# Optimization experiments

Hardware: AMD Instinct MI355X
Metric: run time of the kernel (lower is better)

Reference implementation:

```python
import jax, jax.numpy as jnp
import numpy as np

N = 100_000   # active voxels
CIN = 64
COUT = 64
K = 3
L = 128       # voxel grid extent per axis
C = K // 2    # kernel center


def _offsets():
    # spatial offsets (z, y, x) for all non-center kernel taps, in the same
    # enumeration order as the original module's triple loop
    offs = []
    for dz in range(K):
        for dy in range(K):
            for dx in range(K):
                if (dz, dy, dx) != (C, C, C):
                    offs.append((dz - C, dy - C, dx - C))
    return offs


def _build_neighbor_map(coords):
    # coords: [N,3] int, unique. For each offset build (out_idx, in_idx) pairs
    # where voxel out_idx has an active neighbor in_idx at coords+offset.
    keys = (coords[:, 0].astype(np.int64) * L + coords[:, 1]) * L + coords[:, 2]
    order = np.argsort(keys)
    skeys = keys[order]
    pairs = []
    for (z, y, x) in _offsets():
        nb = coords + np.array([z, y, x], dtype=coords.dtype)
        valid = np.all((nb >= 0) & (nb < L), axis=1)
        nkeys = (nb[:, 0].astype(np.int64) * L + nb[:, 1]) * L + nb[:, 2]
        pos = np.clip(np.searchsorted(skeys, nkeys), 0, N - 1)
        found = valid & (skeys[pos] == nkeys)
        out_idx = np.nonzero(found)[0].astype(np.int32)
        in_idx = order[pos[found]].astype(np.int32)
        pairs.append((out_idx, in_idx))
    P = max(len(o) for o, _ in pairs)
    nei = np.zeros((len(pairs), P, 2), dtype=np.int32)
    sizes = np.zeros(len(pairs), dtype=np.int32)
    for i, (o, j) in enumerate(pairs):
        nei[i, :len(o), 0] = o
        nei[i, :len(o), 1] = j
        sizes[i] = len(o)
    return nei, sizes


def setup_inputs() -> dict:
    rng = np.random.default_rng(0)
    flat = rng.choice(L * L * L, size=N, replace=False)  # unique voxel coords
    coords = np.stack([flat // (L * L), (flat // L) % L, flat % L], axis=1).astype(np.int32)
    nei, sizes = _build_neighbor_map(coords)
    key = jax.random.key(0)
    k1, k2, k3 = jax.random.split(key, 3)
    sp_values = jax.random.normal(k1, (N, CIN), dtype=jnp.float32)
    weight = jax.random.normal(k2, (COUT, K, K, K, CIN), dtype=jnp.float32) * 0.05
    bias = jax.random.normal(k3, (COUT,), dtype=jnp.float32)
    return {"sp_values": sp_values, "weight": weight, "bias": bias,
            "nei_indices": jnp.asarray(nei), "nei_sizes": jnp.asarray(sizes)}


def reference(sp_values, weight, bias, nei_indices, nei_sizes):
    # weight: [Cout,kz,ky,kx,Cin] -> [kz,ky,kx,Cin,Cout] (matches torch permute)
    w = jnp.transpose(weight, (1, 2, 3, 4, 0))
    out = sp_values @ w[C, C, C]                                   # center tap: [N,Cout]
    offs = _offsets()
    w_offs = jnp.stack([w[z + C, y + C, x + C] for (z, y, x) in offs])  # [O,Cin,Cout]
    P = nei_indices.shape[1]
    valid = (jnp.arange(P)[None, :] < nei_sizes[:, None]).astype(sp_values.dtype)  # [O,P]
    gathered = sp_values[nei_indices[:, :, 1]] * valid[:, :, None]  # [O,P,Cin], padded rows zeroed
    contrib = jnp.einsum('opc,ocd->opd', gathered, w_offs)          # [O,P,Cout]
    out = out.at[nei_indices[:, :, 0].reshape(-1)].add(contrib.reshape(-1, out.shape[1]))
    return out + bias
```

## Files before the change

### kernel.cpp

```cpp
#include <hip/hip_runtime.h>
#include <hip/hip_bf16.h>


typedef __bf16 bf16x8 __attribute__((ext_vector_type(8)));
typedef float f32x4 __attribute__((ext_vector_type(4)));

#define TROWS 128
#define WSTR 72

__device__ __forceinline__ unsigned short f2bf(float f) {
    union { float f; unsigned int u; } v; v.f = f;
    unsigned int u = v.u;
    return (unsigned short)((u + 0x7FFFu + ((u >> 16) & 1u)) >> 16);
}
__device__ __forceinline__ ushort4 cvt4(float4 v) {
    ushort4 b;
    b.x = f2bf(v.x); b.y = f2bf(v.y); b.z = f2bf(v.z); b.w = f2bf(v.w);
    return b;
}

__global__ __launch_bounds__(256) void sp3d_prep(
    const float* __restrict__ w, const int* __restrict__ nei,
    const int* __restrict__ sizes, unsigned short* __restrict__ wbf,
    int* __restrict__ starts, int P, int T, int wblocks)
{
    const int b = blockIdx.x;
    if (b < wblocks) {
        int id = b * 256 + threadIdx.x;
        if (id < 27 * 64 * 16) {
            int k4 = id & 15, n = (id >> 4) & 63, tap = id >> 10;
            float4 v = *(const float4*)&w[n * 1728 + tap * 64 + k4 * 4];
            *(ushort4*)&wbf[(tap * 64 + n) * 64 + k4 * 4] = cvt4(v);
        }
    } else {
        int id = (b - wblocks) * 256 + threadIdx.x;
        if (id < 26 * (T + 1)) {
            int t = id % (T + 1), o = id / (T + 1);
            int target = t * TROWS;
            int lo = 0, hi = sizes[o];
            while (lo < hi) {
                int mid = (lo + hi) >> 1;
                if (nei[(o * P + mid) * 2] < target) lo = mid + 1; else hi = mid;
            }
            starts[o * (T + 1) + t] = lo;
        }
    }
}

__device__ __forceinline__ bf16x8 pack8(float4 a, float4 b) {
    union { __hip_bfloat162 h[4]; bf16x8 v; } u;
    u.h[0] = __float22bfloat162_rn(float2{a.x, a.y});
    u.h[1] = __float22bfloat162_rn(float2{a.z, a.w});
    u.h[2] = __float22bfloat162_rn(float2{b.x, b.y});
    u.h[3] = __float22bfloat162_rn(float2{b.z, b.w});
    return u.v;
}

__device__ __forceinline__ void stage_w(unsigned short* dst, const unsigned short* wbf,
                                        int tap, int t) {
    int n = t >> 2, kc = (t & 3) << 4;
    const uint4* src = (const uint4*)&wbf[(tap * 64 + n) * 64 + kc];
    uint4 a = src[0], b = src[1];
    *(uint4*)&dst[n * WSTR + kc] = a;
    *(uint4*)&dst[n * WSTR + kc + 8] = b;
}

__global__ __launch_bounds__(256, 4) void sp3d_main(
    const float* __restrict__ sp, const float* __restrict__ bias,
    const int* __restrict__ nei, const unsigned short* __restrict__ wbf,
    const int* __restrict__ starts, float* __restrict__ out,
    int N, int P, int T)
{
    __shared__ unsigned short Wbuf[2][64 * WSTR];
    __shared__ int tbl[27 * TROWS];
    __shared__ int sOff[27];
    __shared__ int sLo[26];

    const int t = threadIdx.x;
    const int w = t >> 6, lane = t & 63, ml = lane & 15, quad = lane >> 4;
    const int bid = blockIdx.x, row0 = bid * TROWS;

    for (int i = t; i < 27 * TROWS; i += 256) tbl[i] = -1;
    if (t < TROWS) { int r = row0 + t; tbl[13 * TROWS + t] = (r < N) ? r : -1; }
    if (t < 64) {
        int o = t, lo = 0, cnt = 0;
        if (o < 26) {
            lo = starts[o * (T + 1) + bid];
            cnt = starts[o * (T + 1) + bid + 1] - lo;
            sLo[o] = lo;
        }
        int x = cnt;
        #pragma unroll
        for (int d = 1; d < 32; d <<= 1) {
            int y = __shfl_up(x, d);
            if (t >= d) x += y;
        }
        if (o < 26) sOff[o] = x - cnt;
        if (o == 25) sOff[26] = x;
    }
    __syncthreads();
    const int total = sOff[26];
    for (int s = t; s < total; s += 256) {
        int lo = 0, hi = 26;
        while (hi - lo > 1) { int m = (lo + hi) >> 1; if (sOff[m] <= s) lo = m; else hi = m; }
        int o = lo;
        int2 e = *(const int2*)&nei[((long)o * P + sLo[o] + (s - sOff[o])) * 2];
        int tap = o + (o >= 13 ? 1 : 0);
        tbl[tap * TROWS + (e.x - row0)] = e.y;
    }
    stage_w(Wbuf[0], wbf, 0, t);
    __syncthreads();

    f32x4 acc[2][4];
    #pragma unroll
    for (int mt = 0; mt < 2; ++mt)
        #pragma unroll
        for (int nt = 0; nt < 4; ++nt) acc[mt][nt] = f32x4{0.f, 0.f, 0.f, 0.f};

    for (int tap = 0; tap < 27; ++tap) {
        const int cur = tap & 1;
        if (tap + 1 < 27) stage_w(Wbuf[cur ^ 1], wbf, tap + 1, t);

        bf16x8 a[2][2];
        bool act[2];
        #pragma unroll
        for (int mt = 0; mt < 2; ++mt) {
            int idx = tbl[tap * TROWS + w * 32 + mt * 16 + ml];
            act[mt] = __any(idx >= 0);
            if (act[mt]) {
                float4 f0{0,0,0,0}, f1{0,0,0,0}, f2{0,0,0,0}, f3{0,0,0,0};
                if (idx >= 0) {
                    const float* rp = sp + (long)idx * 64 + quad * 8;
                    f0 = *(const float4*)rp;       f1 = *(const float4*)(rp + 4);
                    f2 = *(const float4*)(rp + 32); f3 = *(const float4*)(rp + 36);
                }
                a[mt][0] = pack8(f0, f1);
                a[mt][1] = pack8(f2, f3);
            }
        }
        if (act[0] | act[1]) {
            #pragma unroll
            for (int nt = 0; nt < 4; ++nt) {
                bf16x8 b0 = *(const bf16x8*)&Wbuf[cur][(nt * 16 + ml) * WSTR + quad * 8];
                bf16x8 b1 = *(const bf16x8*)&Wbuf[cur][(nt * 16 + ml) * WSTR + 32 + quad * 8];
                #pragma unroll
                for (int mt = 0; mt < 2; ++mt) {
                    if (act[mt]) {
                        acc[mt][nt] = __builtin_amdgcn_mfma_f32_16x16x32_bf16(a[mt][0], b0, acc[mt][nt], 0, 0, 0);
                        acc[mt][nt] = __builtin_amdgcn_mfma_f32_16x16x32_bf16(a[mt][1], b1, acc[mt][nt], 0, 0, 0);
                    }
                }
            }
        }
        __syncthreads();
    }

    float bv[4];
    #pragma unroll
    for (int nt = 0; nt < 4; ++nt) bv[nt] = bias[nt * 16 + ml];
    #pragma unroll
    for (int mt = 0; mt < 2; ++mt)
        #pragma unroll
        for (int rg = 0; rg < 4; ++rg) {
            long row = row0 + w * 32 + mt * 16 + quad * 4 + rg;
            if (row < N) {
                #pragma unroll
                for (int nt = 0; nt < 4; ++nt)
                    out[row * 64 + nt * 16 + ml] = acc[mt][nt][rg] + bv[nt];
            }
        }
}

extern "C" void kernel_launch(void* const* d_in, const int* in_sizes, int n_in,
                              void* d_out, int out_size, void* d_ws, size_t ws_size,
                              hipStream_t stream) {
    const float* sp    = (const float*)d_in[0];
    const float* w     = (const float*)d_in[1];
    const float* bias  = (const float*)d_in[2];
    const int*   nei   = (const int*)d_in[3];
    const int*   sizes = (const int*)d_in[4];
    float* out = (float*)d_out;

    const int N = in_sizes[0] / 64;
    const int P = in_sizes[3] / 52;
    const int T = (N + TROWS - 1) / TROWS;

    unsigned short* wbf = (unsigned short*)d_ws;
    int* starts = (int*)((char*)d_ws + 27 * 64 * 64 * 2);

    const int wblocks = (27 * 64 * 16 + 255) / 256;
    const int sblocks = (26 * (T + 1) + 255) / 256;
    sp3d_prep<<<wblocks + sblocks, 256, 0, stream>>>(w, nei, sizes, wbf, starts, P, T, wblocks);
    sp3d_main<<<T, 256, 0, stream>>>(sp, bias, nei, wbf, starts, out, N, P, T);
}
```

Baseline: 124.3 us.

## Register double-buffer tap loads, read weights from global, split waves by column

The shared-memory weight double buffer and the per-tap block barrier are removed. Each wave now loads its B fragments straight from global or L2 and keeps two register stages, loading tap k+1 while it runs the MFMAs for tap k. The wave mapping changes from 4 waves x 32 rows x 64 columns to 2 row groups x 2 column halves of 64 rows x 32 columns. The aim is to remove the 27 block barriers and overlap gather latency with compute. In exchange, register pressure rises (occupancy hint drops from 4 to 3), every A gather is now done by two waves, and rows that are all inactive still get loaded and packed.

```diff
diff --git a/kernel.cpp b/kernel.cpp
--- a/kernel.cpp
+++ b/kernel.cpp
@@ -6,7 +6,6 @@
 typedef float f32x4 __attribute__((ext_vector_type(4)));
 
 #define TROWS 128
-#define WSTR 72
 
 __device__ __forceinline__ unsigned short f2bf(float f) {
     union { float f; unsigned int u; } v; v.f = f;
@@ -17,6 +16,14 @@
     ushort4 b;
     b.x = f2bf(v.x); b.y = f2bf(v.y); b.z = f2bf(v.z); b.w = f2bf(v.w);
     return b;
+}
+__device__ __forceinline__ bf16x8 pack8(float4 a, float4 b) {
+    union { __hip_bfloat162 h[4]; bf16x8 v; } u;
+    u.h[0] = __float22bfloat162_rn(float2{a.x, a.y});
+    u.h[1] = __float22bfloat162_rn(float2{a.z, a.w});
+    u.h[2] = __float22bfloat162_rn(float2{b.x, b.y});
+    u.h[3] = __float22bfloat162_rn(float2{b.z, b.w});
+    return u.v;
 }
 
 __global__ __launch_bounds__(256) void sp3d_prep(
@@ -47,38 +54,21 @@
     }
 }
 
-__device__ __forceinline__ bf16x8 pack8(float4 a, float4 b) {
-    union { __hip_bfloat162 h[4]; bf16x8 v; } u;
-    u.h[0] = __float22bfloat162_rn(float2{a.x, a.y});
-    u.h[1] = __float22bfloat162_rn(float2{a.z, a.w});
-    u.h[2] = __float22bfloat162_rn(float2{b.x, b.y});
-    u.h[3] = __float22bfloat162_rn(float2{b.z, b.w});
-    return u.v;
-}
-
-__device__ __forceinline__ void stage_w(unsigned short* dst, const unsigned short* wbf,
-                                        int tap, int t) {
-    int n = t >> 2, kc = (t & 3) << 4;
-    const uint4* src = (const uint4*)&wbf[(tap * 64 + n) * 64 + kc];
-    uint4 a = src[0], b = src[1];
-    *(uint4*)&dst[n * WSTR + kc] = a;
-    *(uint4*)&dst[n * WSTR + kc + 8] = b;
-}
-
-__global__ __launch_bounds__(256, 4) void sp3d_main(
+__global__ __launch_bounds__(256, 3) void sp3d_main(
     const float* __restrict__ sp, const float* __restrict__ bias,
     const int* __restrict__ nei, const unsigned short* __restrict__ wbf,
     const int* __restrict__ starts, float* __restrict__ out,
     int N, int P, int T)
 {
-    __shared__ unsigned short Wbuf[2][64 * WSTR];
     __shared__ int tbl[27 * TROWS];
     __shared__ int sOff[27];
     __shared__ int sLo[26];
 
     const int t = threadIdx.x;
     const int w = t >> 6, lane = t & 63, ml = lane & 15, quad = lane >> 4;
+    const int wrow = w >> 1, ch = w & 1;
     const int bid = blockIdx.x, row0 = bid * TROWS;
+    const __bf16* Wg = (const __bf16*)wbf;
 
     for (int i = t; i < 27 * TROWS; i += 256) tbl[i] = -1;
     if (t < TROWS) { int r = row0 + t; tbl[13 * TROWS + t] = (r < N) ? r : -1; }
@@ -108,65 +98,73 @@
         int tap = o + (o >= 13 ? 1 : 0);
         tbl[tap * TROWS + (e.x - row0)] = e.y;
     }
-    stage_w(Wbuf[0], wbf, 0, t);
     __syncthreads();
 
-    f32x4 acc[2][4];
+    f32x4 acc[4][2];
     #pragma unroll
-    for (int mt = 0; mt < 2; ++mt)
+    for (int mt = 0; mt < 4; ++mt)
         #pragma unroll
-        for (int nt = 0; nt < 4; ++nt) acc[mt][nt] = f32x4{0.f, 0.f, 0.f, 0.f};
+        for (int nt = 0; nt < 2; ++nt) acc[mt][nt] = f32x4{0.f, 0.f, 0.f, 0.f};
 
-    for (int tap = 0; tap < 27; ++tap) {
-        const int cur = tap & 1;
-        if (tap + 1 < 27) stage_w(Wbuf[cur ^ 1], wbf, tap + 1, t);
+    bf16x8 A0[4][2], A1[4][2], B0[2][2], B1[2][2];
+    bool ac0[4], ac1[4];
 
-        bf16x8 a[2][2];
-        bool act[2];
+    auto load_stage = [&](int tap, bf16x8 (&A)[4][2], bf16x8 (&B)[2][2], bool (&ac)[4]) {
         #pragma unroll
-        for (int mt = 0; mt < 2; ++mt) {
-            int idx = tbl[tap * TROWS + w * 32 + mt * 16 + ml];
-            act[mt] = __any(idx >= 0);
-            if (act[mt]) {
-                float4 f0{0,0,0,0}, f1{0,0,0,0}, f2{0,0,0,0}, f3{0,0,0,0};
-                if (idx >= 0) {
-                    const float* rp = sp + (long)idx * 64 + quad * 8;
-                    f0 = *(const float4*)rp;       f1 = *(const float4*)(rp + 4);
-                    f2 = *(const float4*)(rp + 32); f3 = *(const float4*)(rp + 36);
-                }
-                a[mt][0] = pack8(f0, f1);
-                a[mt][1] = pack8(f2, f3);
+        for (int nt = 0; nt < 2; ++nt) {
+            const __bf16* bp = Wg + ((tap * 64 + ch * 32 + nt * 16 + ml) * 64 + quad * 8);
+            B[nt][0] = *(const bf16x8*)bp;
+            B[nt][1] = *(const bf16x8*)(bp + 32);
+        }
+        #pragma unroll
+        for (int mt = 0; mt < 4; ++mt) {
+            int idx = tbl[tap * TROWS + wrow * 64 + mt * 16 + ml];
+            ac[mt] = __any(idx >= 0);
+            float4 f0{0,0,0,0}, f1{0,0,0,0}, f2{0,0,0,0}, f3{0,0,0,0};
+            if (idx >= 0) {
+                const float* rp = sp + (long)idx * 64 + quad * 8;
+                f0 = *(const float4*)rp;        f1 = *(const float4*)(rp + 4);
+                f2 = *(const float4*)(rp + 32); f3 = *(const float4*)(rp + 36);
             }
+            A[mt][0] = pack8(f0, f1);
+            A[mt][1] = pack8(f2, f3);
         }
-        if (act[0] | act[1]) {
-            #pragma unroll
-            for (int nt = 0; nt < 4; ++nt) {
-                bf16x8 b0 = *(const bf16x8*)&Wbuf[cur][(nt * 16 + ml) * WSTR + quad * 8];
-                bf16x8 b1 = *(const bf16x8*)&Wbuf[cur][(nt * 16 + ml) * WSTR + 32 + quad * 8];
+    };
+    auto mfma_stage = [&](bf16x8 (&A)[4][2], bf16x8 (&B)[2][2], bool (&ac)[4]) {
+        #pragma unroll
+        for (int mt = 0; mt < 4; ++mt) {
+            if (ac[mt]) {
                 #pragma unroll
-                for (int mt = 0; mt < 2; ++mt) {
-                    if (act[mt]) {
-                        acc[mt][nt] = __builtin_amdgcn_mfma_f32_16x16x32_bf16(a[mt][0], b0, acc[mt][nt], 0, 0, 0);
-                        acc[mt][nt] = __builtin_amdgcn_mfma_f32_16x16x32_bf16(a[mt][1], b1, acc[mt][nt], 0, 0, 0);
-                    }
+                for (int nt = 0; nt < 2; ++nt) {
+                    acc[mt][nt] = __builtin_amdgcn_mfma_f32_16x16x32_bf16(A[mt][0], B[nt][0], acc[mt][nt], 0, 0, 0);
+                    acc[mt][nt] = __builtin_amdgcn_mfma_f32_16x16x32_bf16(A[mt][1], B[nt][1], acc[mt][nt], 0, 0, 0);
                 }
             }
         }
-        __syncthreads();
+    };
+
+    load_stage(0, A0, B0, ac0);
+    for (int tap = 0; tap < 27; tap += 2) {
+        if (tap + 1 < 27) load_stage(tap + 1, A1, B1, ac1);
+        mfma_stage(A0, B0, ac0);
+        if (tap + 1 < 27) {
+            if (tap + 2 < 27) load_stage(tap + 2, A0, B0, ac0);
+            mfma_stage(A1, B1, ac1);
+        }
     }
 
-    float bv[4];
+    float bv[2];
     #pragma unroll
-    for (int nt = 0; nt < 4; ++nt) bv[nt] = bias[nt * 16 + ml];
+    for (int nt = 0; nt < 2; ++nt) bv[nt] = bias[ch * 32 + nt * 16 + ml];
     #pragma unroll
-    for (int mt = 0; mt < 2; ++mt)
+    for (int mt = 0; mt < 4; ++mt)
         #pragma unroll
         for (int rg = 0; rg < 4; ++rg) {
-            long row = row0 + w * 32 + mt * 16 + quad * 4 + rg;
+            long row = row0 + wrow * 64 + mt * 16 + quad * 4 + rg;
             if (row < N) {
                 #pragma unroll
-                for (int nt = 0; nt < 4; ++nt)
-                    out[row * 64 + nt * 16 + ml] = acc[mt][nt][rg] + bv[nt];
+                for (int nt = 0; nt < 2; ++nt)
+                    out[row * 64 + ch * 32 + nt * 16 + ml] = acc[mt][nt][rg] + bv[nt];
             }
         }
 }
```

Measured after the change: 180.8 us. 1.45x slower.
